# Performance work log

Hardware: AMD Instinct MI355X
Metric: run time of the kernel (lower is better)

## Reference

```python
import jax, jax.numpy as jnp
import numpy as np

N_NODES = 100000
N_EDGES = 1600000
D_IN = 64
D_OUT = 64


def setup_inputs() -> dict:
    key = jax.random.key(0)
    k1, k2, k3 = jax.random.split(key, 3)
    edge_index = jax.random.randint(k1, (2, N_EDGES), 0, N_NODES, dtype=jnp.int64)
    x = jax.random.normal(k2, (N_NODES, D_IN), dtype=jnp.float32)
    W = jax.random.normal(k3, (D_OUT, D_IN), dtype=jnp.float32) * (1.0 / np.sqrt(D_IN))
    return {"edge_index": edge_index, "x": x, "W": W}


def reference(edge_index, x, W):
    # GCN forward: h = W x, then out = D^{-1/2} A D^{-1/2} h (symmetric normalization
    # of the COO edge list, matching normalize_edge_index + CSR SpMM in the original).
    N = x.shape[0]
    row, col = edge_index[0], edge_index[1]
    # degree from row occurrences of the adjacency
    deg = jax.ops.segment_sum(jnp.ones(row.shape, x.dtype), row, num_segments=N)
    dinv_sqrt = jnp.where(deg > 0, 1.0 / jnp.sqrt(deg), 0.0)
    w = dinv_sqrt[row] * dinv_sqrt[col]  # [E] edge weights
    xh = x @ W.T                          # dense linear, bias=False  [N, D_OUT]
    # SpMM: out[r] = sum_e w_e * xh[col_e] for edges with row_e == r
    out = jax.ops.segment_sum(w[:, None] * xh[col], row, num_segments=N)
    return out
```

## Files before the change

### kernel.cpp

```cpp
#include <hip/hip_runtime.h>
#include <hip/hip_fp16.h>

#define D     64
#define RPB   256
#define BCAP  4608
#define EPB   4096
#define NBMAX 400

__global__ __launch_bounds__(256) void bucket_kernel(const int* __restrict__ ei, int E,
                                                     int nb,
                                                     int* __restrict__ cursor,
                                                     int* __restrict__ bbuf) {
    __shared__ int hist[NBMAX];
    __shared__ int base_l[NBMAX];
    __shared__ int stage_v[EPB];
    __shared__ unsigned short stage_b[EPB];
    int tid = threadIdx.x;

    for (int i = tid; i < nb; i += 256) hist[i] = 0;
    __syncthreads();

    long long e0 = (long long)blockIdx.x * EPB;
#pragma unroll
    for (int i = 0; i < EPB / 256; ++i) {
        int idx = i * 256 + tid;
        long long e = e0 + idx;
        unsigned short b = 0xFFFF;
        int v = 0;
        if (e < E) {
            int r = ei[e];
            int c = ei[E + e];
            b = (unsigned short)(r >> 8);
            v = ((r & (RPB - 1)) << 17) | c;
            atomicAdd(&hist[b], 1);
        }
        stage_v[idx] = v;
        stage_b[idx] = b;
    }
    __syncthreads();

    for (int i = tid; i < nb; i += 256) {
        int c = hist[i];
        base_l[i] = (c > 0) ? atomicAdd(&cursor[i], c) : 0;
        hist[i] = 0;
    }
    __syncthreads();

#pragma unroll
    for (int i = 0; i < EPB / 256; ++i) {
        int idx = i * 256 + tid;
        unsigned short b = stage_b[idx];
        if (b != 0xFFFF) {
            int off = base_l[b] + atomicAdd(&hist[b], 1);
            if (off < BCAP)
                bbuf[(size_t)b * BCAP + off] = stage_v[idx];
        }
    }
}

__global__ __launch_bounds__(256) void sort_kernel(const int* __restrict__ cursor,
                                                   int* __restrict__ bbuf,
                                                   float* __restrict__ dinv,
                                                   int2* __restrict__ rowinfo, int N) {
    __shared__ int staged[BCAP];
    __shared__ int sorted[BCAP];
    __shared__ int hist[RPB];
    __shared__ int pfx[RPB];
    __shared__ int curs[RPB];
    int b = blockIdx.x, tid = threadIdx.x;
    int cnt = min(cursor[b], BCAP);
    int* gbuf = bbuf + (size_t)b * BCAP;

    hist[tid] = 0;
    __syncthreads();
    for (int j = tid; j < cnt; j += 256) {
        int v = gbuf[j];
        staged[j] = v;
        atomicAdd(&hist[v >> 17], 1);
    }
    __syncthreads();

    int dv = hist[tid];
    pfx[tid] = dv;
    __syncthreads();
    for (int off = 1; off < 256; off <<= 1) {
        int add = (tid >= off) ? pfx[tid - off] : 0;
        __syncthreads();
        pfx[tid] += add;
        __syncthreads();
    }
    int excl = pfx[tid] - dv;

    int r = (b << 8) + tid;
    if (r < N) {
        dinv[r] = (dv > 0) ? rsqrtf((float)dv) : 0.0f;
        rowinfo[r] = make_int2(b * BCAP + excl, dv);
    }
    curs[tid] = excl;
    __syncthreads();

    for (int j = tid; j < cnt; j += 256) {
        int val = staged[j];
        int pos = atomicAdd(&curs[val >> 17], 1);
        sorted[pos] = val;
    }
    __syncthreads();
    for (int j = tid; j < cnt; j += 256) gbuf[j] = sorted[j];
}

__global__ __launch_bounds__(256) void linear_kernel(const float* __restrict__ x,
                                                     const float* __restrict__ W,
                                                     const float* __restrict__ dinv,
                                                     __half* __restrict__ xh, int N) {
    int c  = threadIdx.x & 63;
    int wl = threadIdx.x >> 6;

    float w[D];
    const float4* W4 = (const float4*)(W + (size_t)c * D);
#pragma unroll
    for (int q = 0; q < D / 4; ++q) {
        float4 t = W4[q];
        w[4 * q + 0] = t.x; w[4 * q + 1] = t.y;
        w[4 * q + 2] = t.z; w[4 * q + 3] = t.w;
    }

    int stride = gridDim.x * 4;
    for (int r = blockIdx.x * 4 + wl; r < N; r += stride) {
        float xv = x[(size_t)r * D + c];
        float a0 = 0.f, a1 = 0.f, a2 = 0.f, a3 = 0.f;
#pragma unroll
        for (int k = 0; k < D; k += 4) {
            a0 = fmaf(__uint_as_float(__builtin_amdgcn_readlane(__float_as_uint(xv), k + 0)), w[k + 0], a0);
            a1 = fmaf(__uint_as_float(__builtin_amdgcn_readlane(__float_as_uint(xv), k + 1)), w[k + 1], a1);
            a2 = fmaf(__uint_as_float(__builtin_amdgcn_readlane(__float_as_uint(xv), k + 2)), w[k + 2], a2);
            a3 = fmaf(__uint_as_float(__builtin_amdgcn_readlane(__float_as_uint(xv), k + 3)), w[k + 3], a3);
        }
        float acc = (a0 + a1) + (a2 + a3);
        xh[(size_t)r * D + c] = __float2half(dinv[r] * acc);
    }
}

__global__ __launch_bounds__(256) void spmm_kernel(const int2* __restrict__ rowinfo,
                                                   const int* __restrict__ bbuf,
                                                   const float* __restrict__ dinv,
                                                   const __half2* __restrict__ xh2,
                                                   float2* __restrict__ out2, int N) {
    int r = (blockIdx.x * 256 + threadIdx.x) >> 6;
    if (r >= N) return;
    int c   = threadIdx.x & 63;
    int sub = c >> 5;
    int f   = c & 31;

    int2 ri   = rowinfo[r];
    int start = ri.x;
    int d     = ri.y;
    float dr  = dinv[r];

    float ax = 0.f, ay = 0.f;
    for (int j0 = 0; j0 < d; j0 += 64) {
        int n = d - j0;
        if (n > 64) n = 64;
        int cn_reg = (c < n) ? (bbuf[start + j0 + c] & 0x1FFFF) : N;
        int n8 = (n + 7) & ~7;
        for (int k = 0; k < n8; k += 8) {
            int e0 = __shfl(cn_reg, k + 0 + sub);
            int e1 = __shfl(cn_reg, k + 2 + sub);
            int e2 = __shfl(cn_reg, k + 4 + sub);
            int e3 = __shfl(cn_reg, k + 6 + sub);
            float2 v0 = __half22float2(xh2[(size_t)e0 * 32 + f]);
            float2 v1 = __half22float2(xh2[(size_t)e1 * 32 + f]);
            float2 v2 = __half22float2(xh2[(size_t)e2 * 32 + f]);
            float2 v3 = __half22float2(xh2[(size_t)e3 * 32 + f]);
            ax += (v0.x + v1.x) + (v2.x + v3.x);
            ay += (v0.y + v1.y) + (v2.y + v3.y);
        }
    }
    float sx = ax + __shfl(ax, c ^ 32);
    float sy = ay + __shfl(ay, c ^ 32);
    if (sub == 0) {
        out2[(size_t)r * 32 + f] = make_float2(dr * sx, dr * sy);
    }
}

extern "C" void kernel_launch(void* const* d_in, const int* in_sizes, int n_in,
                              void* d_out, int out_size, void* d_ws, size_t ws_size,
                              hipStream_t stream) {
    const int*   ei = (const int*)d_in[0];
    const float* x  = (const float*)d_in[1];
    const float* W  = (const float*)d_in[2];
    float* out = (float*)d_out;

    int E  = in_sizes[0] / 2;
    int N  = in_sizes[1] / D;
    int nb = (N + RPB - 1) / RPB;

    char* p = (char*)d_ws;
    size_t off = 0;
    auto take = [&](size_t bytes) -> char* {
        char* cur = p + off;
        off = (off + bytes + 255) & ~(size_t)255;
        return cur;
    };
    float*  dinv    = (float*)take((size_t)N * 4);
    int2*   rowinfo = (int2*)take((size_t)N * 8);
    int*    cursor  = (int*)take((size_t)nb * 4);
    int*    bbuf    = (int*)take((size_t)nb * BCAP * 4);
    __half* xh      = (__half*)take((size_t)(N + 1) * D * 2);
    (void)ws_size;

    hipMemsetAsync(cursor, 0, (size_t)nb * 4, stream);
    hipMemsetAsync(xh + (size_t)N * D, 0, D * sizeof(__half), stream);

    bucket_kernel<<<(E + EPB - 1) / EPB, 256, 0, stream>>>(ei, E, nb, cursor, bbuf);
    sort_kernel<<<nb, 256, 0, stream>>>(cursor, bbuf, dinv, rowinfo, N);
    linear_kernel<<<2048, 256, 0, stream>>>(x, W, dinv, xh, N);
    spmm_kernel<<<(N + 3) / 4, 256, 0, stream>>>(rowinfo, bbuf, dinv,
                                                 (const __half2*)xh, (float2*)out, N);
}
```

Baseline: 193.0 us.

## Use MFMA f16 for the dense linear and trim sort-kernel shared staging

Rewrites the x@W^T linear kernel to run on 16x16x32 f16 MFMA instructions, converting x and W to half precision inside the kernel, in place of per-lane readlane FMA loops. The sort kernel drops its shared staging array and reads the global bucket twice, which cuts LDS use and may raise occupancy. The separate memset of the padding row is folded into the linear kernel, and the linear grid is halved. Rounding x and W to fp16 before the product adds precision loss, and the output stores are scattered 2-byte writes.

```diff
diff --git a/kernel.cpp b/kernel.cpp
--- a/kernel.cpp
+++ b/kernel.cpp
@@ -6,6 +6,9 @@
 #define BCAP  4608
 #define EPB   4096
 #define NBMAX 400
+
+typedef __attribute__((ext_vector_type(8))) _Float16 f16x8;
+typedef __attribute__((ext_vector_type(4))) float    f32x4;
 
 __global__ __launch_bounds__(256) void bucket_kernel(const int* __restrict__ ei, int E,
                                                      int nb,
@@ -62,7 +65,6 @@
                                                    int* __restrict__ bbuf,
                                                    float* __restrict__ dinv,
                                                    int2* __restrict__ rowinfo, int N) {
-    __shared__ int staged[BCAP];
     __shared__ int sorted[BCAP];
     __shared__ int hist[RPB];
     __shared__ int pfx[RPB];
@@ -73,11 +75,7 @@
 
     hist[tid] = 0;
     __syncthreads();
-    for (int j = tid; j < cnt; j += 256) {
-        int v = gbuf[j];
-        staged[j] = v;
-        atomicAdd(&hist[v >> 17], 1);
-    }
+    for (int j = tid; j < cnt; j += 256) atomicAdd(&hist[gbuf[j] >> 17], 1);
     __syncthreads();
 
     int dv = hist[tid];
@@ -100,9 +98,9 @@
     __syncthreads();
 
     for (int j = tid; j < cnt; j += 256) {
-        int val = staged[j];
-        int pos = atomicAdd(&curs[val >> 17], 1);
-        sorted[pos] = val;
+        int v = gbuf[j];
+        int pos = atomicAdd(&curs[v >> 17], 1);
+        sorted[pos] = v;
     }
     __syncthreads();
     for (int j = tid; j < cnt; j += 256) gbuf[j] = sorted[j];
@@ -111,32 +109,62 @@
 __global__ __launch_bounds__(256) void linear_kernel(const float* __restrict__ x,
                                                      const float* __restrict__ W,
                                                      const float* __restrict__ dinv,
-                                                     __half* __restrict__ xh, int N) {
-    int c  = threadIdx.x & 63;
-    int wl = threadIdx.x >> 6;
-
-    float w[D];
-    const float4* W4 = (const float4*)(W + (size_t)c * D);
-#pragma unroll
-    for (int q = 0; q < D / 4; ++q) {
-        float4 t = W4[q];
-        w[4 * q + 0] = t.x; w[4 * q + 1] = t.y;
-        w[4 * q + 2] = t.z; w[4 * q + 3] = t.w;
-    }
-
+                                                     __half* __restrict__ xh, int M) {
+    int tid  = threadIdx.x;
+    int lane = tid & 63;
+    int wv   = tid >> 6;
+    int r16  = lane & 15;
+    int quad = lane >> 4;
+
+    if (blockIdx.x == 0 && tid < D) xh[(size_t)M * D + tid] = __float2half(0.0f);
+
+    f16x8 Bf[4][2];
+#pragma unroll
+    for (int g = 0; g < 4; ++g)
+#pragma unroll
+        for (int s = 0; s < 2; ++s) {
+            const float4* wp = (const float4*)(W + (size_t)(16 * g + r16) * D + 32 * s + quad * 8);
+            float4 w0 = wp[0], w1 = wp[1];
+            f16x8 h;
+            h[0] = (_Float16)w0.x; h[1] = (_Float16)w0.y;
+            h[2] = (_Float16)w0.z; h[3] = (_Float16)w0.w;
+            h[4] = (_Float16)w1.x; h[5] = (_Float16)w1.y;
+            h[6] = (_Float16)w1.z; h[7] = (_Float16)w1.w;
+            Bf[g][s] = h;
+        }
+
+    int ntiles = (M + 15) / 16;
     int stride = gridDim.x * 4;
-    for (int r = blockIdx.x * 4 + wl; r < N; r += stride) {
-        float xv = x[(size_t)r * D + c];
-        float a0 = 0.f, a1 = 0.f, a2 = 0.f, a3 = 0.f;
-#pragma unroll
-        for (int k = 0; k < D; k += 4) {
-            a0 = fmaf(__uint_as_float(__builtin_amdgcn_readlane(__float_as_uint(xv), k + 0)), w[k + 0], a0);
-            a1 = fmaf(__uint_as_float(__builtin_amdgcn_readlane(__float_as_uint(xv), k + 1)), w[k + 1], a1);
-            a2 = fmaf(__uint_as_float(__builtin_amdgcn_readlane(__float_as_uint(xv), k + 2)), w[k + 2], a2);
-            a3 = fmaf(__uint_as_float(__builtin_amdgcn_readlane(__float_as_uint(xv), k + 3)), w[k + 3], a3);
-        }
-        float acc = (a0 + a1) + (a2 + a3);
-        xh[(size_t)r * D + c] = __float2half(dinv[r] * acc);
+    for (int t = blockIdx.x * 4 + wv; t < ntiles; t += stride) {
+        int r0 = t * 16;
+        int ra = min(r0 + r16, M - 1);
+        const float4* xp = (const float4*)(x + (size_t)ra * D + quad * 8);
+        float4 a0 = xp[0], a1 = xp[1], a2 = xp[8], a3 = xp[9];
+        f16x8 A0, A1;
+        A0[0] = (_Float16)a0.x; A0[1] = (_Float16)a0.y; A0[2] = (_Float16)a0.z; A0[3] = (_Float16)a0.w;
+        A0[4] = (_Float16)a1.x; A0[5] = (_Float16)a1.y; A0[6] = (_Float16)a1.z; A0[7] = (_Float16)a1.w;
+        A1[0] = (_Float16)a2.x; A1[1] = (_Float16)a2.y; A1[2] = (_Float16)a2.z; A1[3] = (_Float16)a2.w;
+        A1[4] = (_Float16)a3.x; A1[5] = (_Float16)a3.y; A1[6] = (_Float16)a3.z; A1[7] = (_Float16)a3.w;
+
+        f32x4 acc[4];
+#pragma unroll
+        for (int g = 0; g < 4; ++g) {
+            f32x4 z = {0.f, 0.f, 0.f, 0.f};
+            z = __builtin_amdgcn_mfma_f32_16x16x32_f16(A0, Bf[g][0], z, 0, 0, 0);
+            acc[g] = __builtin_amdgcn_mfma_f32_16x16x32_f16(A1, Bf[g][1], z, 0, 0, 0);
+        }
+
+#pragma unroll
+        for (int reg = 0; reg < 4; ++reg) {
+            int rr = r0 + quad * 4 + reg;
+            if (rr < M) {
+                float dvr = dinv[rr];
+                __half* op = xh + (size_t)rr * D + r16;
+#pragma unroll
+                for (int g = 0; g < 4; ++g)
+                    op[16 * g] = __float2half(dvr * acc[g][reg]);
+            }
+        }
     }
 }
 
@@ -209,11 +237,10 @@
     (void)ws_size;
 
     hipMemsetAsync(cursor, 0, (size_t)nb * 4, stream);
-    hipMemsetAsync(xh + (size_t)N * D, 0, D * sizeof(__half), stream);
 
     bucket_kernel<<<(E + EPB - 1) / EPB, 256, 0, stream>>>(ei, E, nb, cursor, bbuf);
     sort_kernel<<<nb, 256, 0, stream>>>(cursor, bbuf, dinv, rowinfo, N);
-    linear_kernel<<<2048, 256, 0, stream>>>(x, W, dinv, xh, N);
+    linear_kernel<<<1024, 256, 0, stream>>>(x, W, dinv, xh, N);
     spmm_kernel<<<(N + 3) / 4, 256, 0, stream>>>(rowinfo, bbuf, dinv,
                                                  (const __half2*)xh, (float2*)out, N);
 }
```

New measurement: 167.1 us. -13.4%, faster.
